# Performance work log

Measured on AMD Instinct MI355X. Metric: run time of the kernel, lower is better.

Reference implementation:

```python
import jax, jax.numpy as jnp
import numpy as np

B, T, D, H = 2, 2048, 512, 8
HD = D // H


def _mha(x, Wi, bi, Wo, bo):
    # torch nn.MultiheadAttention with q=k=v=x, eval mode (no dropout), batch-first math
    b, t, d = x.shape
    qkv = x @ Wi.T + bi                      # (b,t,3D)
    q, k, v = jnp.split(qkv, 3, axis=-1)
    q = q.reshape(b, t, H, HD)
    k = k.reshape(b, t, H, HD)
    v = v.reshape(b, t, H, HD)
    scores = jnp.einsum('bqhd,bkhd->bhqk', q, k) / jnp.sqrt(jnp.float32(HD))
    attn = jax.nn.softmax(scores, axis=-1)   # (b,H,t,t)
    out = jnp.einsum('bhqk,bkhd->bqhd', attn, v).reshape(b, t, d) @ Wo.T + bo
    return out, attn.mean(axis=1)            # weights averaged over heads, torch default


def _block_ids(t, c):
    # importance score is the constant c at every position (grad of sum == ones)
    cum = jnp.cumsum(jnp.full((t,), c, dtype=jnp.float32))
    frac = cum % 1.0
    boundary = (frac < jnp.roll(frac, 1)).astype(jnp.int32)
    return jnp.cumsum(boundary)              # ids in [0, max_blocks]


def _merge(x, ids, m):
    # segment-mean over dynamic blocks; block id 0 (pre-first-boundary) is dropped, as in torch loop i=1..max
    xm = jnp.moveaxis(x, 1, 0)               # (t,b,d)
    sums = jax.ops.segment_sum(xm, ids, num_segments=m + 1)[1:]              # (m,b,d)
    counts = jax.ops.segment_sum(jnp.ones(ids.shape[0], jnp.float32), ids, num_segments=m + 1)[1:]
    merged = sums / (counts[:, None, None] + 1e-10)
    return jnp.moveaxis(merged, 0, 1), counts


def setup_inputs():
    key = jax.random.key(0)
    ks = jax.random.split(key, 12)
    s = 0.02
    d = {'x': jax.random.normal(ks[0], (B, T, D), jnp.float32)}
    for i, n in enumerate(['char', 'block', 'glob']):
        d[n + '_Wi'] = jax.random.normal(ks[1 + 3 * i], (3 * D, D), jnp.float32) * s
        d[n + '_bi'] = jnp.zeros((3 * D,), jnp.float32)
        d[n + '_Wo'] = jax.random.normal(ks[2 + 3 * i], (D, D), jnp.float32) * s
        d[n + '_bo'] = jnp.zeros((D,), jnp.float32)
    d['merge_w'] = jax.random.normal(ks[10], (D,), jnp.float32) * 0.01
    d['merge_b'] = jnp.array([0.37], jnp.float32)
    d['gmerge_w'] = jax.random.normal(ks[11], (D,), jnp.float32) * 0.01
    d['gmerge_b'] = jnp.array([0.41], jnp.float32)
    return d


def reference(x, char_Wi, char_bi, char_Wo, char_bo, block_Wi, block_bi, block_Wo, block_bo,
              glob_Wi, glob_bi, glob_Wo, glob_bo, merge_w, merge_b, gmerge_w, gmerge_b):
    char_out, char_w = _mha(x, char_Wi, char_bi, char_Wo, char_bo)
    c1 = merge_w.sum() + merge_b[0]
    ids1 = _block_ids(T, c1)
    m1 = int(ids1.max())                      # data-independent given weights; concrete in eager
    blocks, cnt1 = _merge(char_out, ids1, m1)
    block_out, block_w = _mha(blocks, block_Wi, block_bi, block_Wo, block_bo)
    c2 = gmerge_w.sum() + gmerge_b[0]
    ids2 = _block_ids(m1, c2)
    m2 = int(ids2.max())
    glob, cnt2 = _merge(block_out, ids2, m2)
    glob_out, glob_w = _mha(glob, glob_Wi, glob_bi, glob_Wo, glob_bo)
    # double repeat_interleave expansion == gather: token t -> char block -> global block
    ids1n = np.asarray(ids1)
    ids2n = np.asarray(ids2)
    token_g = np.where(ids1n >= 1, ids2n[np.maximum(ids1n - 1, 0)], 0)
    tok_idx = np.nonzero(token_g >= 1)[0]
    expanded = glob_out[:, jnp.asarray(token_g[tok_idx] - 1), :]
    return expanded, char_w, block_w, glob_w
```

## Files before the change

### kernel.cpp

```cpp
#include <hip/hip_runtime.h>
#include <cstdint>
#include <cstddef>


#define TB 2
#define TT 2048
#define TD 512
#define TH 8
#define THD 64
#define KC 4

#define MI_M1 0
#define MI_M2 1
#define MI_NTOK 2
#define MI_OFF_CW 3
#define MI_OFF_BW 4
#define MI_OFF_GW 5
#define MI_MCHAR 6
#define MI_MBLOCK 7
#define MI_MGLOB 8
#define MI_SEQC 9
#define MI_SEQB 10
#define MI_SEQG 11

typedef _Float16 half8 __attribute__((ext_vector_type(8)));
typedef _Float16 half4 __attribute__((ext_vector_type(4)));
typedef _Float16 half2_t __attribute__((ext_vector_type(2)));
typedef float floatx4 __attribute__((ext_vector_type(4)));

__device__ __forceinline__ floatx4 mfma16(half8 a, half8 b, floatx4 c) {
  return __builtin_amdgcn_mfma_f32_16x16x32_f16(a, b, c, 0, 0, 0);
}
__device__ __forceinline__ floatx4 mfma16k16(half4 a, half4 b, floatx4 c) {
  return __builtin_amdgcn_mfma_f32_16x16x16f16(a, b, c, 0, 0, 0);
}

__device__ __forceinline__ void barrier_nodrain() {
  asm volatile("s_waitcnt lgkmcnt(0)" ::: "memory");
  __builtin_amdgcn_s_barrier();
}

__device__ __forceinline__ double fracd(double x) { return x - floor(x); }

__device__ int scan_phase(int n, double c, int* __restrict__ ids,
                          int* __restrict__ startg, float* __restrict__ cntg,
                          int* __restrict__ wsum, int t)
{
  int loc[8];
  const int base = t * 8;
#pragma unroll
  for (int j = 0; j < 8; ++j) {
    const int i = base + j;
    int f = 0;
    if (i < n) {
      const int pidx = (i == 0) ? n : i;
      f = (fracd((double)(i + 1) * c) < fracd((double)pidx * c)) ? 1 : 0;
    }
    loc[j] = f + ((j > 0) ? loc[j - 1] : 0);
  }
  wsum[t] = loc[7];
  __syncthreads();
  for (int off = 1; off < 256; off <<= 1) {
    int u = 0;
    if (t >= off) u = wsum[t - off];
    __syncthreads();
    wsum[t] += u;
    __syncthreads();
  }
  const int excl = wsum[t] - loc[7];
  const int m = wsum[255];
#pragma unroll
  for (int j = 0; j < 8; ++j) {
    const int i = base + j;
    if (i < n) {
      const int id = excl + loc[j];
      ids[i] = id;
      const int f = loc[j] - ((j > 0) ? loc[j - 1] : 0);
      if (f) startg[id - 1] = i;
    }
  }
  __syncthreads();
  for (int j = t; j < m; j += 256)
    cntg[j] = (float)((((j + 1) < m) ? startg[j + 1] : n) - startg[j]);
  __syncthreads();
  return m;
}

__global__ __launch_bounds__(256)
void meta_kernel(const float* __restrict__ mw, const float* __restrict__ mb,
                 const float* __restrict__ gw, const float* __restrict__ gb,
                 int* __restrict__ mi,
                 int* __restrict__ start1, float* __restrict__ cnt1,
                 int* __restrict__ start2, float* __restrict__ cnt2,
                 int* __restrict__ gmap)
{
  __shared__ int ids1[TT];
  __shared__ int ids2[TT];
  __shared__ int wsum[256];
  __shared__ double dsh[256];
  const int t = threadIdx.x;

  double s1 = 0.0, s2 = 0.0;
  for (int i = t; i < TD; i += 256) { s1 += (double)mw[i]; s2 += (double)gw[i]; }
  dsh[t] = s1; __syncthreads();
  for (int off = 128; off > 0; off >>= 1) {
    if (t < off) dsh[t] += dsh[t + off];
    __syncthreads();
  }
  const double c1 = dsh[0] + (double)mb[0];
  __syncthreads();
  dsh[t] = s2; __syncthreads();
  for (int off = 128; off > 0; off >>= 1) {
    if (t < off) dsh[t] += dsh[t + off];
    __syncthreads();
  }
  const double c2 = dsh[0] + (double)gb[0];
  __syncthreads();

  const int m1 = scan_phase(TT, c1, ids1, start1, cnt1, wsum, t);
  const int m2 = scan_phase(m1, c2, ids2, start2, cnt2, wsum, t);

  int i0 = TT;
  if (m1 >= 1 && m2 >= 1) i0 = start1[start2[0]];
  const int ntok = TT - i0;

  if (t == 0) {
    mi[MI_M1] = m1; mi[MI_M2] = m2; mi[MI_NTOK] = ntok;
    const int offcw = TB * ntok * TD;
    mi[MI_OFF_CW] = offcw;
    mi[MI_OFF_BW] = offcw + TB * TT * TT;
    mi[MI_OFF_GW] = offcw + TB * TT * TT + TB * m1 * m1;
    mi[MI_MCHAR] = TB * TT;
    mi[MI_MBLOCK] = TB * m1;
    mi[MI_MGLOB] = TB * m2;
    mi[MI_SEQC] = TT;
    mi[MI_SEQB] = m1;
    mi[MI_SEQG] = m2;
  }
  for (int i = i0 + t; i < TT; i += 256)
    gmap[i - i0] = ids2[ids1[i] - 1] - 1;
}

__global__ __launch_bounds__(256)
void prep_convert(const float* __restrict__ x,
                  const float* __restrict__ wi0, const float* __restrict__ wi1,
                  const float* __restrict__ wi2,
                  const float* __restrict__ wo0, const float* __restrict__ wo1,
                  const float* __restrict__ wo2,
                  _Float16* __restrict__ xh, _Float16* __restrict__ wiH,
                  _Float16* __restrict__ woH, _Float16* __restrict__ woL)
{
  const int r = blockIdx.y;
  const float* src;
  _Float16* dh;
  _Float16* dl = nullptr;
  int n;
  if (r == 0)      { src = x;   dh = xh;                              n = TB * TT * TD; }
  else if (r == 1) { src = wi0; dh = wiH;                             n = 3 * TD * TD; }
  else if (r == 2) { src = wi1; dh = wiH + (size_t)1 * 3 * TD * TD;   n = 3 * TD * TD; }
  else if (r == 3) { src = wi2; dh = wiH + (size_t)2 * 3 * TD * TD;   n = 3 * TD * TD; }
  else if (r == 4) { src = wo0; dh = woH; dl = woL;                   n = TD * TD; }
  else if (r == 5) { src = wo1; dh = woH + (size_t)TD * TD; dl = woL + (size_t)TD * TD; n = TD * TD; }
  else             { src = wo2; dh = woH + (size_t)2 * TD * TD; dl = woL + (size_t)2 * TD * TD; n = TD * TD; }

  const int stride = gridDim.x * 256 * 4;
  for (int i = (blockIdx.x * 256 + threadIdx.x) * 4; i < n; i += stride) {
    const float4 v = *(const float4*)&src[i];
    const float a[4] = {v.x, v.y, v.z, v.w};
    half4 h, l;
#pragma unroll
    for (int e = 0; e < 4; ++e) {
      const _Float16 hh = (_Float16)a[e];
      h[e] = hh;
      l[e] = (_Float16)(a[e] - (float)hh);
    }
    *(half4*)&dh[i] = h;
    if (dl) *(half4*)&dl[i] = l;
  }
}

__global__ __launch_bounds__(256)
void gemm_mfma(const _Float16* __restrict__ A, const _Float16* __restrict__ W,
               const float* __restrict__ bias, _Float16* __restrict__ C,
               const int* __restrict__ mi, int m_slot, int N)
{
  const int M = mi[m_slot];
  const int bm = blockIdx.y * 128;
  if (bm >= M) return;
  const int bn = blockIdx.x * 64;
  __shared__ _Float16 Ah[2][128][40];
  __shared__ _Float16 Wh[2][64][40];

  const int t = threadIdx.x;
  const int wv = t >> 6;
  const int lane = t & 63;
  const int l15 = lane & 15;
  const int quad = lane >> 4;
  const int srowA = t >> 1;
  const int ssegA = (t & 1) * 16;
  const int srowW = t >> 2;
  const int ssegW = (t & 3) * 8;
  const int ar = bm + srowA;
  const size_t abase = (size_t)ar * TD + ssegA;
  const size_t wbase = (size_t)(bn + srowW) * TD + ssegW;

  floatx4 acc[2][4];
#pragma unroll
  for (int i = 0; i < 2; ++i)
#pragma unroll
    for (int j = 0; j < 4; ++j) acc[i][j] = (floatx4){0.f, 0.f, 0.f, 0.f};

  const half8 h8z = {};
  half8 pa0, pa1, pw;

  auto LOADT = [&](int kk) {
    pa0 = h8z; pa1 = h8z;
    if (ar < M) {
      pa0 = *(const half8*)&A[abase + kk];
      pa1 = *(const half8*)&A[abase + kk + 8];
    }
    pw = *(const half8*)&W[wbase + kk];
  };
  auto WRITET = [&](int buf) {
    *(half8*)&Ah[buf][srowA][ssegA] = pa0;
    *(half8*)&Ah[buf][srowA][ssegA + 8] = pa1;
    *(half8*)&Wh[buf][srowW][ssegW] = pw;
  };

  LOADT(0);
  for (int it = 0; it < TD / 32; ++it) {
    const int buf = it & 1;
    WRITET(buf);
    if (it + 1 < TD / 32) LOADT((it + 1) * 32);
    barrier_nodrain();
    half8 ah[2];
#pragma unroll
    for (int mp = 0; mp < 2; ++mp)
      ah[mp] = *(const half8*)&Ah[buf][wv * 32 + mp * 16 + l15][quad * 8];
#pragma unroll
    for (int np = 0; np < 4; ++np) {
      const half8 bh = *(const half8*)&Wh[buf][np * 16 + l15][quad * 8];
#pragma unroll
      for (int mp = 0; mp < 2; ++mp)
        acc[mp][np] = mfma16(ah[mp], bh, acc[mp][np]);
    }
  }
  float bv[4];
#pragma unroll
  for (int np = 0; np < 4; ++np) bv[np] = bias[bn + np * 16 + l15];
#pragma unroll
  for (int mp = 0; mp < 2; ++mp) {
#pragma unroll
    for (int r = 0; r < 4; ++r) {
      const int row = bm + wv * 32 + mp * 16 + quad * 4 + r;
      if (row < M) {
        _Float16* cp = &C[(size_t)row * N + bn];
#pragma unroll
        for (int np = 0; np < 4; ++np)
          cp[np * 16 + l15] = (_Float16)(acc[mp][np][r] + bv[np]);
      }
    }
  }
}

__global__ __launch_bounds__(256)
void gemm_norm_mfma(const _Float16* __restrict__ Ob, const float* __restrict__ lb,
                    const _Float16* __restrict__ Whg, const _Float16* __restrict__ Wlg,
                    const float* __restrict__ bias,
                    float* __restrict__ C, const int* __restrict__ mi,
                    int m_slot, int seq_slot)
{
  const int M = mi[m_slot];
  const int bm = blockIdx.y * 64;
  if (bm >= M) return;
  const int seq = mi[seq_slot];
  const int bn = blockIdx.x * 64;
  __shared__ _Float16 Ah[2][64][40];
  __shared__ _Float16 Al[2][64][40];
  __shared__ _Float16 Wh[2][64][40];
  __shared__ _Float16 Wl[2][64][40];

  const int t = threadIdx.x;
  const int wv = t >> 6;
  const int lane = t & 63;
  const int l15 = lane & 15;
  const int quad = lane >> 4;
  const int srow = t >> 2;
  const int sseg = (t & 3) * 8;

  const int ar = bm + srow;
  const int ab = (ar >= seq) ? 1 : 0;
  const int aq = ar - ab * seq;
  const size_t wbase = (size_t)(bn + srow) * TD + sseg;

  floatx4 acc[4];
#pragma unroll
  for (int j = 0; j < 4; ++j) acc[j] = (floatx4){0.f, 0.f, 0.f, 0.f};

  const half8 h8z = {};
  half8 pOb[KC];
  float plb[KC];
  half8 pwh, pwl;

  auto LOADT = [&](int kk) {
    if (ar < M) {
      const size_t off = (size_t)ar * TD + kk + sseg;
#pragma unroll
      for (int z = 0; z < KC; ++z)
        pOb[z] = *(const half8*)&Ob[(size_t)z * 2097152 + off];
      const int h = kk >> 6;
      const size_t lidx = ((size_t)(ab * TH + h)) * 2048 + aq;
#pragma unroll
      for (int z = 0; z < KC; ++z) plb[z] = lb[(size_t)z * 32768 + lidx];
    } else {
#pragma unroll
      for (int z = 0; z < KC; ++z) { pOb[z] = h8z; plb[z] = 1.f; }
    }
    pwh = *(const half8*)&Whg[wbase + kk];
    pwl = *(const half8*)&Wlg[wbase + kk];
  };
  auto WRITET = [&](int buf) {
    float aa[8] = {0.f, 0.f, 0.f, 0.f, 0.f, 0.f, 0.f, 0.f};
    if (ar < M) {
#pragma unroll
      for (int z = 0; z < KC; ++z)
#pragma unroll
        for (int e = 0; e < 8; ++e) aa[e] += (float)pOb[z][e];
      const float lt = plb[0] + plb[1] + plb[2] + plb[3];
      const float linv = 1.f / lt;
#pragma unroll
      for (int e = 0; e < 8; ++e) aa[e] *= linv;
    }
    half8 hi, lo;
#pragma unroll
    for (int e = 0; e < 8; ++e) {
      const _Float16 h = (_Float16)aa[e];
      hi[e] = h; lo[e] = (_Float16)(aa[e] - (float)h);
    }
    *(half8*)&Ah[buf][srow][sseg] = hi;
    *(half8*)&Al[buf][srow][sseg] = lo;
    *(half8*)&Wh[buf][srow][sseg] = pwh;
    *(half8*)&Wl[buf][srow][sseg] = pwl;
  };

  LOADT(0);
  for (int it = 0; it < TD / 32; ++it) {
    const int buf = it & 1;
    WRITET(buf);
    if (it + 1 < TD / 32) LOADT((it + 1) * 32);
    barrier_nodrain();
    const half8 ah = *(const half8*)&Ah[buf][wv * 16 + l15][quad * 8];
    const half8 al = *(const half8*)&Al[buf][wv * 16 + l15][quad * 8];
#pragma unroll
    for (int np = 0; np < 4; ++np) {
      const half8 bh = *(const half8*)&Wh[buf][np * 16 + l15][quad * 8];
      const half8 bl = *(const half8*)&Wl[buf][np * 16 + l15][quad * 8];
      acc[np] = mfma16(al, bh, acc[np]);
      acc[np] = mfma16(ah, bl, acc[np]);
      acc[np] = mfma16(ah, bh, acc[np]);
    }
  }
  float bv[4];
#pragma unroll
  for (int np = 0; np < 4; ++np) bv[np] = bias[bn + np * 16 + l15];
#pragma unroll
  for (int r = 0; r < 4; ++r) {
    const int row = bm + wv * 16 + quad * 4 + r;
    if (row < M) {
      float* cp = &C[(size_t)row * 512 + bn];
#pragma unroll
      for (int np = 0; np < 4; ++np)
        cp[np * 16 + l15] = acc[np][r] + bv[np];
    }
  }
}

__global__ __launch_bounds__(256)
void attn1_mfma(const _Float16* __restrict__ qkv,
                float* __restrict__ lbase, _Float16* __restrict__ Obase,
                const int* __restrict__ mi, int seq_slot)
{
  const int seq = mi[seq_slot];
  const int q0 = blockIdx.x * 128;
  if (q0 >= seq) return;
  const int b = blockIdx.y >> 3, h = blockIdx.y & 7;
  const int z = blockIdx.z;
  float* lP = lbase + (size_t)z * 32768;
  _Float16* oP = Obase + (size_t)z * 2097152;
  const int t = threadIdx.x;
  const int wv = t >> 6;
  const int lane = t & 63;
  const int l15 = lane & 15;
  const int quad = lane >> 4;

  __shared__ __align__(16) char smem_raw[36864];
  float (*Ot)[68] = (float (*)[68])smem_raw;

  half8 qB[2][2];
#pragma unroll
  for (int mp = 0; mp < 2; ++mp) {
    const int qrow = q0 + wv * 32 + mp * 16 + l15;
#pragma unroll
    for (int c = 0; c < 2; ++c) {
      half8 v = {};
      if (qrow < seq)
        v = *(const half8*)&qkv[((size_t)(b * seq + qrow)) * 1536 + h * 64 + c * 32 + quad * 8];
      qB[mp][c] = v;
    }
  }
  half4 onesA;
#pragma unroll
  for (int j = 0; j < 4; ++j) onesA[j] = (_Float16)1.0f;

  floatx4 oacc[2][4];
#pragma unroll
  for (int i = 0; i < 2; ++i)
#pragma unroll
    for (int j = 0; j < 4; ++j) oacc[i][j] = (floatx4){0.f, 0.f, 0.f, 0.f};
  floatx4 lacc[2] = {(floatx4){0.f, 0.f, 0.f, 0.f}, (floatx4){0.f, 0.f, 0.f, 0.f}};

  const int nkt = (seq + 63) >> 6;
  const int nkc = (nkt + KC - 1) / KC;
  const int kt_beg = z * nkc;
  const int kt_end = min(kt_beg + nkc, nkt);

  const int krow = t >> 2;
  const int kseg = (t & 3) * 16;
  const int tp = lane & 31;
  const int dsel = lane >> 5;
  const int dbase = wv * 16 + dsel * 8;

  const half8 h8z = {};
  half8 pk0, pk1, pva, pvb;

  auto LOADKV = [&](int kt) {
    const int k0 = kt * 64;
    pk0 = h8z; pk1 = h8z; pva = h8z; pvb = h8z;
    const int kg = k0 + krow;
    if (kg < seq) {
      const _Float16* base = &qkv[((size_t)(b * seq + kg)) * 1536 + 512 + h * 64 + kseg];
      pk0 = *(const half8*)base;
      pk1 = *(const half8*)(base + 8);
    }
    const int kg0 = k0 + tp * 2;
    if (kg0 < seq)
      pva = *(const half8*)&qkv[((size_t)(b * seq + kg0)) * 1536 + 1024 + h * 64 + dbase];
    if (kg0 + 1 < seq)
      pvb = *(const half8*)&qkv[((size_t)(b * seq + kg0 + 1)) * 1536 + 1024 + h * 64 + dbase];
  };

  LOADKV(kt_beg);
  for (int kt = kt_beg; kt < kt_end; ++kt) {
    char* sb = smem_raw + (size_t)((kt - kt_beg) & 1) * 18432;
    _Float16 (*Kf)[72] = (_Float16 (*)[72])sb;
    _Float16 (*Vt)[72] = (_Float16 (*)[72])(sb + 9216);

    *(half8*)&Kf[krow][kseg] = pk0;
    *(half8*)&Kf[krow][kseg + 8] = pk1;
#pragma unroll
    for (int j = 0; j < 8; ++j) {
      half2_t pkk; pkk[0] = pva[j]; pkk[1] = pvb[j];
      *(half2_t*)&Vt[dbase + j][tp * 2] = pkk;
    }
    if (kt + 1 < kt_end) LOADKV(kt + 1);
    barrier_nodrain();

    const int k0 = kt * 64;
    const bool kfull = (k0 + 64 <= seq);
#pragma unroll
    for (int p = 0; p < 4; ++p) {
      floatx4 sT[2] = {(floatx4){0.f, 0.f, 0.f, 0.f}, (floatx4){0.f, 0.f, 0.f, 0.f}};
#pragma unroll
      for (int c = 0; c < 2; ++c) {
        const half8 kA = *(const half8*)&Kf[p * 16 + l15][c * 32 + quad * 8];
#pragma unroll
        for (int mp = 0; mp < 2; ++mp)
          sT[mp] = mfma16(kA, qB[mp][c], sT[mp]);
      }
      half4 vA[4];
#pragma unroll
      for (int dblk = 0; dblk < 4; ++dblk)
        vA[dblk] = *(const half4*)&Vt[dblk * 16 + l15][p * 16 + quad * 4];
      const int kg = k0 + p * 16 + quad * 4;
#pragma unroll
      for (int mp = 0; mp < 2; ++mp) {
        half4 eB;
        if (kfull) {
#pragma unroll
          for (int r = 0; r < 4; ++r)
            eB[r] = (_Float16)__expf(sT[mp][r] * 0.125f);
        } else {
#pragma unroll
          for (int r = 0; r < 4; ++r) {
            const float e = (kg + r < seq) ? __expf(sT[mp][r] * 0.125f) : 0.f;
            eB[r] = (_Float16)e;
          }
        }
        lacc[mp] = mfma16k16(onesA, eB, lacc[mp]);
#pragma unroll
        for (int dblk = 0; dblk < 4; ++dblk)
          oacc[mp][dblk] = mfma16k16(vA[dblk], eB, oacc[mp][dblk]);
      }
    }
  }

  __syncthreads();

#pragma unroll
  for (int mp = 0; mp < 2; ++mp) {
#pragma unroll
    for (int dblk = 0; dblk < 4; ++dblk)
      *(floatx4*)&Ot[wv * 16 + l15][dblk * 16 + quad * 4] = oacc[mp][dblk];
    const int ql = lane >> 2;
    const int dseg = (lane & 3) * 4;
    const int qg = q0 + wv * 32 + mp * 16 + ql;
    if (qg < seq) {
      _Float16* op = &oP[((size_t)(b * seq + qg)) * 512 + h * 64];
#pragma unroll
      for (int u = 0; u < 4; ++u) {
        const float4 v = *(const float4*)&Ot[wv * 16 + ql][u * 16 + dseg];
        half4 hv;
        hv[0] = (_Float16)v.x; hv[1] = (_Float16)v.y;
        hv[2] = (_Float16)v.z; hv[3] = (_Float16)v.w;
        *(half4*)(op + u * 16 + dseg) = hv;
      }
    }
    if (quad == 0) {
      const int qg2 = q0 + wv * 32 + mp * 16 + l15;
      if (qg2 < seq)
        lP[((size_t)(b * TH + h)) * 2048 + qg2] = lacc[mp][0];
    }
  }
}

__global__ __launch_bounds__(256)
void attn2_mfma(const _Float16* __restrict__ qkv,
                const float* __restrict__ lb,
                float* __restrict__ outb, const int* __restrict__ mi,
                int seq_slot, int off_slot)
{
  const int seq = mi[seq_slot];
  const int q0 = blockIdx.y * 64;
  const int k0 = blockIdx.x * 128;
  if (q0 >= seq || k0 >= seq) return;
  const int b = blockIdx.z;
  const int woff = mi[off_slot];
  float* wout = outb + (size_t)woff + (size_t)b * seq * seq;

  __shared__ _Float16 Ksh[2][128][72];
  __shared__ float Linv8[TH][64];

  const int t = threadIdx.x;
  const int wv = t >> 6;
  const int lane = t & 63;
  const int l15 = lane & 15;
  const int quad = lane >> 4;
  const int srowK = t >> 1;
  const int ssegK = (t & 1) * 32;

  for (int i = t; i < TH * 64; i += 256) {
    const int hh = i >> 6;
    const int qq = i & 63;
    float lv = 1.f;
    if (q0 + qq < seq) {
      const size_t lidx = ((size_t)(b * TH + hh)) * 2048 + q0 + qq;
      float lt = 0.f;
#pragma unroll
      for (int zz = 0; zz < KC; ++zz) lt += lb[(size_t)zz * 32768 + lidx];
      lv = lt;
    }
    Linv8[hh][qq] = 1.f / lv;
  }

  floatx4 acc[8];
#pragma unroll
  for (int j = 0; j < 8; ++j) acc[j] = (floatx4){0.f, 0.f, 0.f, 0.f};

  const int qr = q0 + wv * 16 + l15;
  const int kr = k0 + srowK;
  const bool qok = (qr < seq);
  const bool kok = (kr < seq);
  const size_t qoff = (size_t)(b * seq + qr) * 1536 + quad * 8;
  const size_t koff = (size_t)(b * seq + kr) * 1536 + 512 + ssegK;

  const half8 h8z = {};
  half8 pk[4];
  half8 qcur0, qcur1, qnxt0, qnxt1;

  auto LOADK = [&](int h) {
#pragma unroll
    for (int u = 0; u < 4; ++u) {
      pk[u] = h8z;
      if (kok) pk[u] = *(const half8*)&qkv[koff + h * 64 + u * 8];
    }
  };
  auto LOADQ = [&](int h, half8& d0, half8& d1) {
    d0 = h8z; d1 = h8z;
    if (qok) {
      d0 = *(const half8*)&qkv[qoff + h * 64];
      d1 = *(const half8*)&qkv[qoff + h * 64 + 32];
    }
  };

  LOADK(0);
  LOADQ(0, qcur0, qcur1);
  for (int h = 0; h < TH; ++h) {
    const int buf = h & 1;
#pragma unroll
    for (int u = 0; u < 4; ++u)
      *(half8*)&Ksh[buf][srowK][ssegK + u * 8] = pk[u];
    if (h + 1 < TH) { LOADK(h + 1); LOADQ(h + 1, qnxt0, qnxt1); }
    barrier_nodrain();

    float lv[4];
#pragma unroll
    for (int r = 0; r < 4; ++r)
      lv[r] = Linv8[h][wv * 16 + quad * 4 + r];

#pragma unroll
    for (int np = 0; np < 8; ++np) {
      const half8 bf0 = *(const half8*)&Ksh[buf][np * 16 + l15][quad * 8];
      const half8 bf1 = *(const half8*)&Ksh[buf][np * 16 + l15][32 + quad * 8];
      floatx4 s = (floatx4){0.f, 0.f, 0.f, 0.f};
      s = mfma16(qcur0, bf0, s);
      s = mfma16(qcur1, bf1, s);
#pragma unroll
      for (int r = 0; r < 4; ++r)
        acc[np][r] += __expf(s[r] * 0.125f) * lv[r];
    }
    qcur0 = qnxt0; qcur1 = qnxt1;
  }

#pragma unroll
  for (int r = 0; r < 4; ++r) {
    const int qg = q0 + wv * 16 + quad * 4 + r;
    if (qg >= seq) continue;
    float* rowp = wout + (size_t)qg * seq;
#pragma unroll
    for (int np = 0; np < 8; ++np) {
      const int col = k0 + np * 16 + l15;
      if (col < seq) rowp[col] = acc[np][r] * 0.125f;
    }
  }
}

__global__ __launch_bounds__(256)
void merge_kernel(const float* __restrict__ src, _Float16* __restrict__ dst,
                  const int* __restrict__ start, const float* __restrict__ cnt,
                  const int* __restrict__ mi, int seqin_slot, int seqout_slot)
{
  const int j = blockIdx.x;
  const int b = blockIdx.y;
  const int seqo = mi[seqout_slot];
  if (j >= seqo) return;
  const int seqi = mi[seqin_slot];
  const int s = start[j];
  const float cf = cnt[j];
  const int n = (int)cf;
  const int d0 = threadIdx.x * 2;
  float s0 = 0.f, s1 = 0.f;
  const float* p = &src[((size_t)b * seqi + s) * TD + d0];
  for (int i = 0; i < n; ++i) {
    const float2 v = *(const float2*)p;
    s0 += v.x; s1 += v.y;
    p += TD;
  }
  const float inv = 1.f / (cf + 1e-10f);
  half2_t o;
  o[0] = (_Float16)(s0 * inv);
  o[1] = (_Float16)(s1 * inv);
  *(half2_t*)&dst[((size_t)b * seqo + j) * TD + d0] = o;
}

__global__ __launch_bounds__(256)
void expand_kernel(const float* __restrict__ gout, float* __restrict__ dout,
                   const int* __restrict__ gmap, const int* __restrict__ mi)
{
  const int j = blockIdx.x;
  const int b = blockIdx.y;
  const int ntok = mi[MI_NTOK];
  if (j >= ntok) return;
  const int m2 = mi[MI_M2];
  const int g = gmap[j];
  const int d0 = threadIdx.x * 2;
  const float2 v = *(const float2*)&gout[((size_t)b * m2 + g) * TD + d0];
  *(float2*)&dout[((size_t)b * ntok + j) * TD + d0] = v;
}

extern "C" void kernel_launch(void* const* d_in, const int* in_sizes, int n_in,
                              void* d_out, int out_size, void* d_ws, size_t ws_size,
                              hipStream_t stream)
{
  const float* x   = (const float*)d_in[0];
  const float* cWi = (const float*)d_in[1];
  const float* cbi = (const float*)d_in[2];
  const float* cWo = (const float*)d_in[3];
  const float* cbo = (const float*)d_in[4];
  const float* bWi = (const float*)d_in[5];
  const float* bbi = (const float*)d_in[6];
  const float* bWo = (const float*)d_in[7];
  const float* bbo = (const float*)d_in[8];
  const float* gWi = (const float*)d_in[9];
  const float* gbi = (const float*)d_in[10];
  const float* gWo = (const float*)d_in[11];
  const float* gbo = (const float*)d_in[12];
  const float* mw  = (const float*)d_in[13];
  const float* mbv = (const float*)d_in[14];
  const float* gw  = (const float*)d_in[15];
  const float* gbv = (const float*)d_in[16];
  float* outf = (float*)d_out;

  char* wsb = (char*)d_ws;
  int*   mi     = (int*)(wsb);
  int*   start1 = (int*)(wsb + 1024);
  float* cnt1   = (float*)(wsb + 1024 + 8192);
  int*   start2 = (int*)(wsb + 1024 + 2 * 8192);
  float* cnt2   = (float*)(wsb + 1024 + 3 * 8192);
  int*   gmap   = (int*)(wsb + 1024 + 4 * 8192);
  float* lbase  = (float*)(wsb + 65536);
  _Float16* qkv = (_Float16*)(wsb + 655360);
  _Float16* Obase = (_Float16*)(wsb + 655360 + 12582912);
  float* stg_o  = (float*)(wsb + 30015488);
  _Float16* stg_mh = (_Float16*)(wsb + 38404096);
  _Float16* xh  = (_Float16*)(wsb + 42598400);
  _Float16* wiH = (_Float16*)(wsb + 46792704);
  _Float16* woH = (_Float16*)(wsb + 51511296);
  _Float16* woL = (_Float16*)(wsb + 53084160);

  const dim3 blk(256);

  meta_kernel<<<dim3(1), blk, 0, stream>>>(mw, mbv, gw, gbv, mi, start1, cnt1, start2, cnt2, gmap);
  prep_convert<<<dim3(256, 7), blk, 0, stream>>>(x, cWi, bWi, gWi, cWo, bWo, gWo,
                                                 xh, wiH, woH, woL);

  gemm_mfma<<<dim3(24, 32), blk, 0, stream>>>(xh, wiH, cbi, qkv, mi, MI_MCHAR, 1536);
  attn1_mfma<<<dim3(16, 16, KC), blk, 0, stream>>>(qkv, lbase, Obase, mi, MI_SEQC);
  attn2_mfma<<<dim3(16, 32, 2), blk, 0, stream>>>(qkv, lbase, outf, mi, MI_SEQC, MI_OFF_CW);
  gemm_norm_mfma<<<dim3(8, 64), blk, 0, stream>>>(Obase, lbase, woH, woL, cbo, stg_o, mi, MI_MCHAR, MI_SEQC);
  merge_kernel<<<dim3(2048, 2), blk, 0, stream>>>(stg_o, stg_mh, start1, cnt1, mi, MI_SEQC, MI_SEQB);

  gemm_mfma<<<dim3(24, 32), blk, 0, stream>>>(stg_mh, wiH + (size_t)786432, bbi, qkv, mi, MI_MBLOCK, 1536);
  attn1_mfma<<<dim3(16, 16, KC), blk, 0, stream>>>(qkv, lbase, Obase, mi, MI_SEQB);
  attn2_mfma<<<dim3(16, 32, 2), blk, 0, stream>>>(qkv, lbase, outf, mi, MI_SEQB, MI_OFF_BW);
  gemm_norm_mfma<<<dim3(8, 64), blk, 0, stream>>>(Obase, lbase, woH + (size_t)262144, woL + (size_t)262144, bbo, stg_o, mi, MI_MBLOCK, MI_SEQB);
  merge_kernel<<<dim3(2048, 2), blk, 0, stream>>>(stg_o, stg_mh, start2, cnt2, mi, MI_SEQB, MI_SEQG);

  gemm_mfma<<<dim3(24, 32), blk, 0, stream>>>(stg_mh, wiH + (size_t)2 * 786432, gbi, qkv, mi, MI_MGLOB, 1536);
  attn1_mfma<<<dim3(16, 16, KC), blk, 0, stream>>>(qkv, lbase, Obase, mi, MI_SEQG);
  attn2_mfma<<<dim3(16, 32, 2), blk, 0, stream>>>(qkv, lbase, outf, mi, MI_SEQG, MI_OFF_GW);
  gemm_norm_mfma<<<dim3(8, 64), blk, 0, stream>>>(Obase, lbase, woH + (size_t)2 * 262144, woL + (size_t)2 * 262144, gbo, stg_o, mi, MI_MGLOB, MI_SEQG);
  expand_kernel<<<dim3(2048, 2), blk, 0, stream>>>(stg_o, outf, gmap, mi);

  (void)in_sizes; (void)n_in; (void)out_size; (void)ws_size;
}
```

Measured before the change: 332.8 us.

## Merge independent kernels via blockIdx dispatch and fold softmax scale into Q projection

```diff
diff --git a/kernel.cpp b/kernel.cpp
--- a/kernel.cpp
+++ b/kernel.cpp
@@ -87,12 +87,19 @@
 }
 
 __global__ __launch_bounds__(256)
-void meta_kernel(const float* __restrict__ mw, const float* __restrict__ mb,
-                 const float* __restrict__ gw, const float* __restrict__ gb,
-                 int* __restrict__ mi,
-                 int* __restrict__ start1, float* __restrict__ cnt1,
-                 int* __restrict__ start2, float* __restrict__ cnt2,
-                 int* __restrict__ gmap)
+void meta_prep(const float* __restrict__ mw, const float* __restrict__ mb,
+               const float* __restrict__ gw, const float* __restrict__ gb,
+               int* __restrict__ mi,
+               int* __restrict__ start1, float* __restrict__ cnt1,
+               int* __restrict__ start2, float* __restrict__ cnt2,
+               int* __restrict__ gmap,
+               const float* __restrict__ x,
+               const float* __restrict__ wi0, const float* __restrict__ wi1,
+               const float* __restrict__ wi2,
+               const float* __restrict__ wo0, const float* __restrict__ wo1,
+               const float* __restrict__ wo2,
+               _Float16* __restrict__ xh, _Float16* __restrict__ wiH,
+               _Float16* __restrict__ woH, _Float16* __restrict__ woL)
 {
   __shared__ int ids1[TT];
   __shared__ int ids2[TT];
@@ -100,56 +107,50 @@
   __shared__ double dsh[256];
   const int t = threadIdx.x;
 
-  double s1 = 0.0, s2 = 0.0;
-  for (int i = t; i < TD; i += 256) { s1 += (double)mw[i]; s2 += (double)gw[i]; }
-  dsh[t] = s1; __syncthreads();
-  for (int off = 128; off > 0; off >>= 1) {
-    if (t < off) dsh[t] += dsh[t + off];
+  if (blockIdx.y == 7) {
+    if (blockIdx.x != 0) return;
+    double s1 = 0.0, s2 = 0.0;
+    for (int i = t; i < TD; i += 256) { s1 += (double)mw[i]; s2 += (double)gw[i]; }
+    dsh[t] = s1; __syncthreads();
+    for (int off = 128; off > 0; off >>= 1) {
+      if (t < off) dsh[t] += dsh[t + off];
+      __syncthreads();
+    }
+    const double c1 = dsh[0] + (double)mb[0];
     __syncthreads();
-  }
-  const double c1 = dsh[0] + (double)mb[0];
-  __syncthreads();
-  dsh[t] = s2; __syncthreads();
-  for (int off = 128; off > 0; off >>= 1) {
-    if (t < off) dsh[t] += dsh[t + off];
+    dsh[t] = s2; __syncthreads();
+    for (int off = 128; off > 0; off >>= 1) {
+      if (t < off) dsh[t] += dsh[t + off];
+      __syncthreads();
+    }
+    const double c2 = dsh[0] + (double)gb[0];
     __syncthreads();
-  }
-  const double c2 = dsh[0] + (double)gb[0];
-  __syncthreads();
-
-  const int m1 = scan_phase(TT, c1, ids1, start1, cnt1, wsum, t);
-  const int m2 = scan_phase(m1, c2, ids2, start2, cnt2, wsum, t);
-
-  int i0 = TT;
-  if (m1 >= 1 && m2 >= 1) i0 = start1[start2[0]];
-  const int ntok = TT - i0;
-
-  if (t == 0) {
-    mi[MI_M1] = m1; mi[MI_M2] = m2; mi[MI_NTOK] = ntok;
-    const int offcw = TB * ntok * TD;
-    mi[MI_OFF_CW] = offcw;
-    mi[MI_OFF_BW] = offcw + TB * TT * TT;
-    mi[MI_OFF_GW] = offcw + TB * TT * TT + TB * m1 * m1;
-    mi[MI_MCHAR] = TB * TT;
-    mi[MI_MBLOCK] = TB * m1;
-    mi[MI_MGLOB] = TB * m2;
-    mi[MI_SEQC] = TT;
-    mi[MI_SEQB] = m1;
-    mi[MI_SEQG] = m2;
-  }
-  for (int i = i0 + t; i < TT; i += 256)
-    gmap[i - i0] = ids2[ids1[i] - 1] - 1;
-}
-
-__global__ __launch_bounds__(256)
-void prep_convert(const float* __restrict__ x,
-                  const float* __restrict__ wi0, const float* __restrict__ wi1,
-                  const float* __restrict__ wi2,
-                  const float* __restrict__ wo0, const float* __restrict__ wo1,
-                  const float* __restrict__ wo2,
-                  _Float16* __restrict__ xh, _Float16* __restrict__ wiH,
-                  _Float16* __restrict__ woH, _Float16* __restrict__ woL)
-{
+
+    const int m1 = scan_phase(TT, c1, ids1, start1, cnt1, wsum, t);
+    const int m2 = scan_phase(m1, c2, ids2, start2, cnt2, wsum, t);
+
+    int i0 = TT;
+    if (m1 >= 1 && m2 >= 1) i0 = start1[start2[0]];
+    const int ntok = TT - i0;
+
+    if (t == 0) {
+      mi[MI_M1] = m1; mi[MI_M2] = m2; mi[MI_NTOK] = ntok;
+      const int offcw = TB * ntok * TD;
+      mi[MI_OFF_CW] = offcw;
+      mi[MI_OFF_BW] = offcw + TB * TT * TT;
+      mi[MI_OFF_GW] = offcw + TB * TT * TT + TB * m1 * m1;
+      mi[MI_MCHAR] = TB * TT;
+      mi[MI_MBLOCK] = TB * m1;
+      mi[MI_MGLOB] = TB * m2;
+      mi[MI_SEQC] = TT;
+      mi[MI_SEQB] = m1;
+      mi[MI_SEQG] = m2;
+    }
+    for (int i = i0 + t; i < TT; i += 256)
+      gmap[i - i0] = ids2[ids1[i] - 1] - 1;
+    return;
+  }
+
   const int r = blockIdx.y;
   const float* src;
   _Float16* dh;
@@ -245,6 +246,7 @@
         acc[mp][np] = mfma16(ah[mp], bh, acc[mp][np]);
     }
   }
+  const float qs = (bn < 512) ? 0.125f : 1.0f;
   float bv[4];
 #pragma unroll
   for (int np = 0; np < 4; ++np) bv[np] = bias[bn + np * 16 + l15];
@@ -257,120 +259,8 @@
         _Float16* cp = &C[(size_t)row * N + bn];
 #pragma unroll
         for (int np = 0; np < 4; ++np)
-          cp[np * 16 + l15] = (_Float16)(acc[mp][np][r] + bv[np]);
-      }
-    }
-  }
-}
-
-__global__ __launch_bounds__(256)
-void gemm_norm_mfma(const _Float16* __restrict__ Ob, const float* __restrict__ lb,
-                    const _Float16* __restrict__ Whg, const _Float16* __restrict__ Wlg,
-                    const float* __restrict__ bias,
-                    float* __restrict__ C, const int* __restrict__ mi,
-                    int m_slot, int seq_slot)
-{
-  const int M = mi[m_slot];
-  const int bm = blockIdx.y * 64;
-  if (bm >= M) return;
-  const int seq = mi[seq_slot];
-  const int bn = blockIdx.x * 64;
-  __shared__ _Float16 Ah[2][64][40];
-  __shared__ _Float16 Al[2][64][40];
-  __shared__ _Float16 Wh[2][64][40];
-  __shared__ _Float16 Wl[2][64][40];
-
-  const int t = threadIdx.x;
-  const int wv = t >> 6;
-  const int lane = t & 63;
-  const int l15 = lane & 15;
-  const int quad = lane >> 4;
-  const int srow = t >> 2;
-  const int sseg = (t & 3) * 8;
-
-  const int ar = bm + srow;
-  const int ab = (ar >= seq) ? 1 : 0;
-  const int aq = ar - ab * seq;
-  const size_t wbase = (size_t)(bn + srow) * TD + sseg;
-
-  floatx4 acc[4];
-#pragma unroll
-  for (int j = 0; j < 4; ++j) acc[j] = (floatx4){0.f, 0.f, 0.f, 0.f};
-
-  const half8 h8z = {};
-  half8 pOb[KC];
-  float plb[KC];
-  half8 pwh, pwl;
-
-  auto LOADT = [&](int kk) {
-    if (ar < M) {
-      const size_t off = (size_t)ar * TD + kk + sseg;
-#pragma unroll
-      for (int z = 0; z < KC; ++z)
-        pOb[z] = *(const half8*)&Ob[(size_t)z * 2097152 + off];
-      const int h = kk >> 6;
-      const size_t lidx = ((size_t)(ab * TH + h)) * 2048 + aq;
-#pragma unroll
-      for (int z = 0; z < KC; ++z) plb[z] = lb[(size_t)z * 32768 + lidx];
-    } else {
-#pragma unroll
-      for (int z = 0; z < KC; ++z) { pOb[z] = h8z; plb[z] = 1.f; }
-    }
-    pwh = *(const half8*)&Whg[wbase + kk];
-    pwl = *(const half8*)&Wlg[wbase + kk];
-  };
-  auto WRITET = [&](int buf) {
-    float aa[8] = {0.f, 0.f, 0.f, 0.f, 0.f, 0.f, 0.f, 0.f};
-    if (ar < M) {
-#pragma unroll
-      for (int z = 0; z < KC; ++z)
-#pragma unroll
-        for (int e = 0; e < 8; ++e) aa[e] += (float)pOb[z][e];
-      const float lt = plb[0] + plb[1] + plb[2] + plb[3];
-      const float linv = 1.f / lt;
-#pragma unroll
-      for (int e = 0; e < 8; ++e) aa[e] *= linv;
-    }
-    half8 hi, lo;
-#pragma unroll
-    for (int e = 0; e < 8; ++e) {
-      const _Float16 h = (_Float16)aa[e];
-      hi[e] = h; lo[e] = (_Float16)(aa[e] - (float)h);
-    }
-    *(half8*)&Ah[buf][srow][sseg] = hi;
-    *(half8*)&Al[buf][srow][sseg] = lo;
-    *(half8*)&Wh[buf][srow][sseg] = pwh;
-    *(half8*)&Wl[buf][srow][sseg] = pwl;
-  };
-
-  LOADT(0);
-  for (int it = 0; it < TD / 32; ++it) {
-    const int buf = it & 1;
-    WRITET(buf);
-    if (it + 1 < TD / 32) LOADT((it + 1) * 32);
-    barrier_nodrain();
-    const half8 ah = *(const half8*)&Ah[buf][wv * 16 + l15][quad * 8];
-    const half8 al = *(const half8*)&Al[buf][wv * 16 + l15][quad * 8];
-#pragma unroll
-    for (int np = 0; np < 4; ++np) {
-      const half8 bh = *(const half8*)&Wh[buf][np * 16 + l15][quad * 8];
-      const half8 bl = *(const half8*)&Wl[buf][np * 16 + l15][quad * 8];
-      acc[np] = mfma16(al, bh, acc[np]);
-      acc[np] = mfma16(ah, bl, acc[np]);
-      acc[np] = mfma16(ah, bh, acc[np]);
-    }
-  }
-  float bv[4];
-#pragma unroll
-  for (int np = 0; np < 4; ++np) bv[np] = bias[bn + np * 16 + l15];
-#pragma unroll
-  for (int r = 0; r < 4; ++r) {
-    const int row = bm + wv * 16 + quad * 4 + r;
-    if (row < M) {
-      float* cp = &C[(size_t)row * 512 + bn];
-#pragma unroll
-      for (int np = 0; np < 4; ++np)
-        cp[np * 16 + l15] = acc[np][r] + bv[np];
+          cp[np * 16 + l15] = (_Float16)((acc[mp][np][r] + bv[np]) * qs);
+      }
     }
   }
 }
@@ -488,11 +378,11 @@
         if (kfull) {
 #pragma unroll
           for (int r = 0; r < 4; ++r)
-            eB[r] = (_Float16)__expf(sT[mp][r] * 0.125f);
+            eB[r] = (_Float16)__expf(sT[mp][r]);
         } else {
 #pragma unroll
           for (int r = 0; r < 4; ++r) {
-            const float e = (kg + r < seq) ? __expf(sT[mp][r] * 0.125f) : 0.f;
+            const float e = (kg + r < seq) ? __expf(sT[mp][r]) : 0.f;
             eB[r] = (_Float16)e;
           }
         }
@@ -534,112 +424,222 @@
 }
 
 __global__ __launch_bounds__(256)
-void attn2_mfma(const _Float16* __restrict__ qkv,
-                const float* __restrict__ lb,
-                float* __restrict__ outb, const int* __restrict__ mi,
-                int seq_slot, int off_slot)
+void attn2norm_mfma(const _Float16* __restrict__ qkv,
+                    const float* __restrict__ lb,
+                    float* __restrict__ outb,
+                    const _Float16* __restrict__ Ob,
+                    const _Float16* __restrict__ Whg, const _Float16* __restrict__ Wlg,
+                    const float* __restrict__ bias,
+                    float* __restrict__ C,
+                    const int* __restrict__ mi,
+                    int seq_slot, int off_slot, int m_slot)
 {
-  const int seq = mi[seq_slot];
-  const int q0 = blockIdx.y * 64;
-  const int k0 = blockIdx.x * 128;
-  if (q0 >= seq || k0 >= seq) return;
-  const int b = blockIdx.z;
-  const int woff = mi[off_slot];
-  float* wout = outb + (size_t)woff + (size_t)b * seq * seq;
-
-  __shared__ _Float16 Ksh[2][128][72];
-  __shared__ float Linv8[TH][64];
-
+  __shared__ __align__(16) char usm[40960];
+  const int bx = blockIdx.x;
   const int t = threadIdx.x;
   const int wv = t >> 6;
   const int lane = t & 63;
   const int l15 = lane & 15;
   const int quad = lane >> 4;
-  const int srowK = t >> 1;
-  const int ssegK = (t & 1) * 32;
-
-  for (int i = t; i < TH * 64; i += 256) {
-    const int hh = i >> 6;
-    const int qq = i & 63;
-    float lv = 1.f;
-    if (q0 + qq < seq) {
-      const size_t lidx = ((size_t)(b * TH + hh)) * 2048 + q0 + qq;
-      float lt = 0.f;
-#pragma unroll
-      for (int zz = 0; zz < KC; ++zz) lt += lb[(size_t)zz * 32768 + lidx];
-      lv = lt;
-    }
-    Linv8[hh][qq] = 1.f / lv;
-  }
-
-  floatx4 acc[8];
-#pragma unroll
-  for (int j = 0; j < 8; ++j) acc[j] = (floatx4){0.f, 0.f, 0.f, 0.f};
-
-  const int qr = q0 + wv * 16 + l15;
-  const int kr = k0 + srowK;
-  const bool qok = (qr < seq);
-  const bool kok = (kr < seq);
-  const size_t qoff = (size_t)(b * seq + qr) * 1536 + quad * 8;
-  const size_t koff = (size_t)(b * seq + kr) * 1536 + 512 + ssegK;
-
-  const half8 h8z = {};
-  half8 pk[4];
-  half8 qcur0, qcur1, qnxt0, qnxt1;
-
-  auto LOADK = [&](int h) {
-#pragma unroll
-    for (int u = 0; u < 4; ++u) {
-      pk[u] = h8z;
-      if (kok) pk[u] = *(const half8*)&qkv[koff + h * 64 + u * 8];
-    }
-  };
-  auto LOADQ = [&](int h, half8& d0, half8& d1) {
-    d0 = h8z; d1 = h8z;
-    if (qok) {
-      d0 = *(const half8*)&qkv[qoff + h * 64];
-      d1 = *(const half8*)&qkv[qoff + h * 64 + 32];
-    }
-  };
-
-  LOADK(0);
-  LOADQ(0, qcur0, qcur1);
-  for (int h = 0; h < TH; ++h) {
-    const int buf = h & 1;
-#pragma unroll
-    for (int u = 0; u < 4; ++u)
-      *(half8*)&Ksh[buf][srowK][ssegK + u * 8] = pk[u];
-    if (h + 1 < TH) { LOADK(h + 1); LOADQ(h + 1, qnxt0, qnxt1); }
-    barrier_nodrain();
-
-    float lv[4];
-#pragma unroll
-    for (int r = 0; r < 4; ++r)
-      lv[r] = Linv8[h][wv * 16 + quad * 4 + r];
-
-#pragma unroll
-    for (int np = 0; np < 8; ++np) {
-      const half8 bf0 = *(const half8*)&Ksh[buf][np * 16 + l15][quad * 8];
-      const half8 bf1 = *(const half8*)&Ksh[buf][np * 16 + l15][32 + quad * 8];
-      floatx4 s = (floatx4){0.f, 0.f, 0.f, 0.f};
-      s = mfma16(qcur0, bf0, s);
-      s = mfma16(qcur1, bf1, s);
+  const int seq = mi[seq_slot];
+
+  if (bx < 1024) {
+    const int k0 = (bx & 15) * 128;
+    const int q0 = ((bx >> 4) & 31) * 64;
+    const int b = bx >> 9;
+    if (q0 >= seq || k0 >= seq) return;
+    const int woff = mi[off_slot];
+    float* wout = outb + (size_t)woff + (size_t)b * seq * seq;
+
+    _Float16 (*Ksh)[128][72] = (_Float16 (*)[128][72])usm;
+    float (*Linv8)[64] = (float (*)[64])(usm + 36864);
+
+    const int srowK = t >> 1;
+    const int ssegK = (t & 1) * 32;
+
+    for (int i = t; i < TH * 64; i += 256) {
+      const int hh = i >> 6;
+      const int qq = i & 63;
+      float lv = 1.f;
+      if (q0 + qq < seq) {
+        const size_t lidx = ((size_t)(b * TH + hh)) * 2048 + q0 + qq;
+        float lt = 0.f;
+#pragma unroll
+        for (int zz = 0; zz < KC; ++zz) lt += lb[(size_t)zz * 32768 + lidx];
+        lv = lt;
+      }
+      Linv8[hh][qq] = 1.f / lv;
+    }
+
+    floatx4 acc[8];
+#pragma unroll
+    for (int j = 0; j < 8; ++j) acc[j] = (floatx4){0.f, 0.f, 0.f, 0.f};
+
+    const int qr = q0 + wv * 16 + l15;
+    const int kr = k0 + srowK;
+    const bool qok = (qr < seq);
+    const bool kok = (kr < seq);
+    const size_t qoff = (size_t)(b * seq + qr) * 1536 + quad * 8;
+    const size_t koff = (size_t)(b * seq + kr) * 1536 + 512 + ssegK;
+
+    const half8 h8z = {};
+    half8 pk[4];
+    half8 qcur0, qcur1, qnxt0, qnxt1;
+
+    auto LOADK = [&](int h) {
+#pragma unroll
+      for (int u = 0; u < 4; ++u) {
+        pk[u] = h8z;
+        if (kok) pk[u] = *(const half8*)&qkv[koff + h * 64 + u * 8];
+      }
+    };
+    auto LOADQ = [&](int h, half8& d0, half8& d1) {
+      d0 = h8z; d1 = h8z;
+      if (qok) {
+        d0 = *(const half8*)&qkv[qoff + h * 64];
+        d1 = *(const half8*)&qkv[qoff + h * 64 + 32];
+      }
+    };
+
+    LOADK(0);
+    LOADQ(0, qcur0, qcur1);
+    for (int h = 0; h < TH; ++h) {
+      const int buf = h & 1;
+#pragma unroll
+      for (int u = 0; u < 4; ++u)
+        *(half8*)&Ksh[buf][srowK][ssegK + u * 8] = pk[u];
+      if (h + 1 < TH) { LOADK(h + 1); LOADQ(h + 1, qnxt0, qnxt1); }
+      barrier_nodrain();
+
+      float lv[4];
 #pragma unroll
       for (int r = 0; r < 4; ++r)
-        acc[np][r] += __expf(s[r] * 0.125f) * lv[r];
-    }
-    qcur0 = qnxt0; qcur1 = qnxt1;
-  }
-
-#pragma unroll
-  for (int r = 0; r < 4; ++r) {
-    const int qg = q0 + wv * 16 + quad * 4 + r;
-    if (qg >= seq) continue;
-    float* rowp = wout + (size_t)qg * seq;
-#pragma unroll
-    for (int np = 0; np < 8; ++np) {
-      const int col = k0 + np * 16 + l15;
-      if (col < seq) rowp[col] = acc[np][r] * 0.125f;
+        lv[r] = Linv8[h][wv * 16 + quad * 4 + r];
+
+#pragma unroll
+      for (int np = 0; np < 8; ++np) {
+        const half8 bf0 = *(const half8*)&Ksh[buf][np * 16 + l15][quad * 8];
+        const half8 bf1 = *(const half8*)&Ksh[buf][np * 16 + l15][32 + quad * 8];
+        floatx4 s = (floatx4){0.f, 0.f, 0.f, 0.f};
+        s = mfma16(qcur0, bf0, s);
+        s = mfma16(qcur1, bf1, s);
+#pragma unroll
+        for (int r = 0; r < 4; ++r)
+          acc[np][r] += __expf(s[r]) * lv[r];
+      }
+      qcur0 = qnxt0; qcur1 = qnxt1;
+    }
+
+#pragma unroll
+    for (int r = 0; r < 4; ++r) {
+      const int qg = q0 + wv * 16 + quad * 4 + r;
+      if (qg >= seq) continue;
+      float* rowp = wout + (size_t)qg * seq;
+#pragma unroll
+      for (int np = 0; np < 8; ++np) {
+        const int col = k0 + np * 16 + l15;
+        if (col < seq) rowp[col] = acc[np][r] * 0.125f;
+      }
+    }
+  } else {
+    const int g = bx - 1024;
+    const int bn = (g & 7) * 64;
+    const int bm = (g >> 3) * 64;
+    const int M = mi[m_slot];
+    if (bm >= M) return;
+
+    _Float16 (*Ah)[64][40] = (_Float16 (*)[64][40])usm;
+    _Float16 (*Al)[64][40] = (_Float16 (*)[64][40])(usm + 10240);
+    _Float16 (*Wh)[64][40] = (_Float16 (*)[64][40])(usm + 20480);
+    _Float16 (*Wl)[64][40] = (_Float16 (*)[64][40])(usm + 30720);
+
+    const int srow = t >> 2;
+    const int sseg = (t & 3) * 8;
+
+    const int ar = bm + srow;
+    const int ab = (ar >= seq) ? 1 : 0;
+    const int aq = ar - ab * seq;
+    const size_t wbase = (size_t)(bn + srow) * TD + sseg;
+
+    floatx4 acc[4];
+#pragma unroll
+    for (int j = 0; j < 4; ++j) acc[j] = (floatx4){0.f, 0.f, 0.f, 0.f};
+
+    const half8 h8z = {};
+    half8 pOb[KC];
+    float plb[KC];
+    half8 pwh, pwl;
+
+    auto LOADT = [&](int kk) {
+      if (ar < M) {
+        const size_t off = (size_t)ar * TD + kk + sseg;
+#pragma unroll
+        for (int z = 0; z < KC; ++z)
+          pOb[z] = *(const half8*)&Ob[(size_t)z * 2097152 + off];
+        const int h = kk >> 6;
+        const size_t lidx = ((size_t)(ab * TH + h)) * 2048 + aq;
+#pragma unroll
+        for (int z = 0; z < KC; ++z) plb[z] = lb[(size_t)z * 32768 + lidx];
+      } else {
+#pragma unroll
+        for (int z = 0; z < KC; ++z) { pOb[z] = h8z; plb[z] = 1.f; }
+      }
+      pwh = *(const half8*)&Whg[wbase + kk];
+      pwl = *(const half8*)&Wlg[wbase + kk];
+    };
+    auto WRITET = [&](int buf) {
+      float aa[8] = {0.f, 0.f, 0.f, 0.f, 0.f, 0.f, 0.f, 0.f};
+      if (ar < M) {
+#pragma unroll
+        for (int z = 0; z < KC; ++z)
+#pragma unroll
+          for (int e = 0; e < 8; ++e) aa[e] += (float)pOb[z][e];
+        const float lt = plb[0] + plb[1] + plb[2] + plb[3];
+        const float linv = 1.f / lt;
+#pragma unroll
+        for (int e = 0; e < 8; ++e) aa[e] *= linv;
+      }
+      half8 hi, lo;
+#pragma unroll
+      for (int e = 0; e < 8; ++e) {
+        const _Float16 h = (_Float16)aa[e];
+        hi[e] = h; lo[e] = (_Float16)(aa[e] - (float)h);
+      }
+      *(half8*)&Ah[buf][srow][sseg] = hi;
+      *(half8*)&Al[buf][srow][sseg] = lo;
+      *(half8*)&Wh[buf][srow][sseg] = pwh;
+      *(half8*)&Wl[buf][srow][sseg] = pwl;
+    };
+
+    LOADT(0);
+    for (int it = 0; it < TD / 32; ++it) {
+      const int buf = it & 1;
+      WRITET(buf);
+      if (it + 1 < TD / 32) LOADT((it + 1) * 32);
+      barrier_nodrain();
+      const half8 ah = *(const half8*)&Ah[buf][wv * 16 + l15][quad * 8];
+      const half8 al = *(const half8*)&Al[buf][wv * 16 + l15][quad * 8];
+#pragma unroll
+      for (int np = 0; np < 4; ++np) {
+        const half8 bh = *(const half8*)&Wh[buf][np * 16 + l15][quad * 8];
+        const half8 bl = *(const half8*)&Wl[buf][np * 16 + l15][quad * 8];
+        acc[np] = mfma16(al, bh, acc[np]);
+        acc[np] = mfma16(ah, bl, acc[np]);
+        acc[np] = mfma16(ah, bh, acc[np]);
+      }
+    }
+    float bv[4];
+#pragma unroll
+    for (int np = 0; np < 4; ++np) bv[np] = bias[bn + np * 16 + l15];
+#pragma unroll
+    for (int r = 0; r < 4; ++r) {
+      const int row = bm + wv * 16 + quad * 4 + r;
+      if (row < M) {
+        float* cp = &C[(size_t)row * 512 + bn];
+#pragma unroll
+        for (int np = 0; np < 4; ++np)
+          cp[np * 16 + l15] = acc[np][r] + bv[np];
+      }
     }
   }
 }
@@ -729,26 +729,29 @@
 
   const dim3 blk(256);
 
-  meta_kernel<<<dim3(1), blk, 0, stream>>>(mw, mbv, gw, gbv, mi, start1, cnt1, start2, cnt2, gmap);
-  prep_convert<<<dim3(256, 7), blk, 0, stream>>>(x, cWi, bWi, gWi, cWo, bWo, gWo,
-                                                 xh, wiH, woH, woL);
+  meta_prep<<<dim3(256, 8), blk, 0, stream>>>(mw, mbv, gw, gbv, mi, start1, cnt1,
+                                              start2, cnt2, gmap,
+                                              x, cWi, bWi, gWi, cWo, bWo, gWo,
+                                              xh, wiH, woH, woL);
 
   gemm_mfma<<<dim3(24, 32), blk, 0, stream>>>(xh, wiH, cbi, qkv, mi, MI_MCHAR, 1536);
   attn1_mfma<<<dim3(16, 16, KC), blk, 0, stream>>>(qkv, lbase, Obase, mi, MI_SEQC);
-  attn2_mfma<<<dim3(16, 32, 2), blk, 0, stream>>>(qkv, lbase, outf, mi, MI_SEQC, MI_OFF_CW);
-  gemm_norm_mfma<<<dim3(8, 64), blk, 0, stream>>>(Obase, lbase, woH, woL, cbo, stg_o, mi, MI_MCHAR, MI_SEQC);
+  attn2norm_mfma<<<dim3(1536), blk, 0, stream>>>(qkv, lbase, outf, Obase, woH, woL, cbo,
+                                                 stg_o, mi, MI_SEQC, MI_OFF_CW, MI_MCHAR);
   merge_kernel<<<dim3(2048, 2), blk, 0, stream>>>(stg_o, stg_mh, start1, cnt1, mi, MI_SEQC, MI_SEQB);
 
   gemm_mfma<<<dim3(24, 32), blk, 0, stream>>>(stg_mh, wiH + (size_t)786432, bbi, qkv, mi, MI_MBLOCK, 1536);
   attn1_mfma<<<dim3(16, 16, KC), blk, 0, stream>>>(qkv, lbase, Obase, mi, MI_SEQB);
-  attn2_mfma<<<dim3(16, 32, 2), blk, 0, stream>>>(qkv, lbase, outf, mi, MI_SEQB, MI_OFF_BW);
-  gemm_norm_mfma<<<dim3(8, 64), blk, 0, stream>>>(Obase, lbase, woH + (size_t)262144, woL + (size_t)262144, bbo, stg_o, mi, MI_MBLOCK, MI_SEQB);
+  attn2norm_mfma<<<dim3(1536), blk, 0, stream>>>(qkv, lbase, outf, Obase,
+                                                 woH + (size_t)262144, woL + (size_t)262144, bbo,
+                                                 stg_o, mi, MI_SEQB, MI_OFF_BW, MI_MBLOCK);
   merge_kernel<<<dim3(2048, 2), blk, 0, stream>>>(stg_o, stg_mh, start2, cnt2, mi, MI_SEQB, MI_SEQG);
 
   gemm_mfma<<<dim3(24, 32), blk, 0, stream>>>(stg_mh, wiH + (size_t)2 * 786432, gbi, qkv, mi, MI_MGLOB, 1536);
   attn1_mfma<<<dim3(16, 16, KC), blk, 0, stream>>>(qkv, lbase, Obase, mi, MI_SEQG);
-  attn2_mfma<<<dim3(16, 32, 2), blk, 0, stream>>>(qkv, lbase, outf, mi, MI_SEQG, MI_OFF_GW);
-  gemm_norm_mfma<<<dim3(8, 64), blk, 0, stream>>>(Obase, lbase, woH + (size_t)2 * 262144, woL + (size_t)2 * 262144, gbo, stg_o, mi, MI_MGLOB, MI_SEQG);
+  attn2norm_mfma<<<dim3(1536), blk, 0, stream>>>(qkv, lbase, outf, Obase,
+                                                 woH + (size_t)2 * 262144, woL + (size_t)2 * 262144, gbo,
+                                                 stg_o, mi, MI_SEQG, MI_OFF_GW, MI_MGLOB);
   expand_kernel<<<dim3(2048, 2), blk, 0, stream>>>(stg_o, outf, gmap, mi);
 
   (void)in_sizes; (void)n_in; (void)out_size; (void)ws_size;
```

Result: slower. 344.2 us (+3.4%).
